# Kernel optimization log

Hardware: AMD Instinct MI355X
Metric: run time of the kernel (lower is better)

The kernel has to match this reference:

```python
import jax, jax.numpy as jnp
import numpy as np

N = 100000
E = 1250000
D = 64
R = 16


def _glorot(key, shape):
    fan_in, fan_out = shape[-2], shape[-1]
    lim = jnp.sqrt(6.0 / (fan_in + fan_out))
    return jax.random.uniform(key, shape, jnp.float32, -lim, lim)


def setup_inputs() -> dict:
    key = jax.random.key(0)
    ks = jax.random.split(key, 9)
    x = jax.random.normal(ks[0], (N, D), jnp.float32)
    edge_index = jax.random.randint(ks[1], (2, E), 0, N, jnp.int64 if jax.config.jax_enable_x64 else jnp.int32).astype(jnp.int32)
    edge_type = jax.random.randint(ks[2], (E,), 0, R).astype(jnp.int32)
    return {
        "x": x,
        "edge_index": edge_index,
        "edge_type": edge_type,
        "W1": _glorot(ks[3], (R, D, D)),
        "sw1": _glorot(ks[4], (D, D)),
        "b1": jnp.zeros((D,), jnp.float32),
        "W2": _glorot(ks[5], (R, D, D)),
        "sw2": _glorot(ks[6], (D, D)),
        "b2": jnp.zeros((D,), jnp.float32),
    }


def _rgcn_layer(x, src, dst, edge_type, W, sw, b, residual):
    # self transform [N, O]
    out = x @ sw
    # per-relation transform of all nodes: [N, R, O] (avoids [E, D, O] gathered weights,
    # same math as bmm(x_j, W[edge_type]))
    xW = jnp.einsum('nd,rdo->nro', x, W)
    msg = xW[src, edge_type]                      # [E, O] per-edge messages
    agg = jax.ops.segment_sum(msg, dst, num_segments=N)  # scatter-add aggregate
    out = out + agg
    if residual:
        out = out + x  # Identity residual (in == out channels)
    out = out + b
    return jax.nn.relu(out)


def reference(x, edge_index, edge_type, W1, sw1, b1, W2, sw2, b2):
    src, dst = edge_index[0], edge_index[1]
    # layer 1: residual=True; layer 2: encoding=False -> no residual.
    # activation (relu) applied after every layer by RGCN.forward; dropout p=0 / eval -> no-op.
    h = _rgcn_layer(x, src, dst, edge_type, W1, sw1, b1, residual=True)
    h = _rgcn_layer(h, src, dst, edge_type, W2, sw2, b2, residual=False)
    return h
```

## Files before the change

kernel.cpp:

```cpp
#include <hip/hip_runtime.h>
#include <hip/hip_bf16.h>

#define NN 100000
#define NE 1250000
#define DD 64
#define RR 16
#define NTILE 6250
#define NBINS 100000
#define NBLK_SCAN 391
#define EBCAP 512

typedef __attribute__((ext_vector_type(8))) short s16x8;
typedef __attribute__((ext_vector_type(4))) float f32x4;

static __device__ __forceinline__ unsigned short f2bf(float v) {
    __hip_bfloat16 h = __float2bfloat16(v);
    return __builtin_bit_cast(unsigned short, h);
}
static __device__ __forceinline__ unsigned int pack2(float a, float b) {
    return ((unsigned int)f2bf(b) << 16) | (unsigned int)f2bf(a);
}


__global__ void hist_key(const int* __restrict__ dst, const int* __restrict__ et,
                         int* __restrict__ cnt) {
    int e = blockIdx.x * 256 + threadIdx.x;
    if (e < NE) atomicAdd(&cnt[(dst[e] >> 4) * 16 + et[e]], 1);
}

__global__ __launch_bounds__(256) void scan1(const int* __restrict__ cnt,
                                             int* __restrict__ rp, int* __restrict__ part) {
    __shared__ int s[256];
    int i = blockIdx.x * 256 + threadIdx.x;
    int v = (i < NBINS) ? cnt[i] : 0;
    s[threadIdx.x] = v;
    __syncthreads();
    for (int off = 1; off < 256; off <<= 1) {
        int t = (threadIdx.x >= off) ? s[threadIdx.x - off] : 0;
        __syncthreads();
        s[threadIdx.x] += t;
        __syncthreads();
    }
    if (i < NBINS) rp[i] = s[threadIdx.x] - v;
    if (threadIdx.x == 255) part[blockIdx.x] = s[255];
}

__global__ void scan2(int* __restrict__ part, int* __restrict__ rp) {
    __shared__ int s[NBLK_SCAN];
    if (threadIdx.x < NBLK_SCAN) s[threadIdx.x] = part[threadIdx.x];
    __syncthreads();
    if (threadIdx.x == 0) {
        int acc = 0;
        for (int b = 0; b < NBLK_SCAN; ++b) { int t = s[b]; s[b] = acc; acc += t; }
        rp[NBINS] = NE;
    }
    __syncthreads();
    if (threadIdx.x < NBLK_SCAN) part[threadIdx.x] = s[threadIdx.x];
}

__global__ void scan3(int* __restrict__ rp, const int* __restrict__ part, int* __restrict__ cur) {
    int i = blockIdx.x * 256 + threadIdx.x;
    if (i < NBINS) {
        int v = rp[i] + part[blockIdx.x];
        rp[i] = v;
        cur[i] = v;
    }
}

__global__ void scatter_key(const int* __restrict__ src, const int* __restrict__ dst,
                            const int* __restrict__ et, int* __restrict__ cur,
                            unsigned int* __restrict__ ep) {
    int e = blockIdx.x * 256 + threadIdx.x;
    if (e >= NE) return;
    int d = dst[e];
    int p = atomicAdd(&cur[(d >> 4) * 16 + et[e]], 1);
    ep[p] = (unsigned int)src[e] | ((unsigned int)(d & 15) << 20);
}


__global__ void prep_w2(const float* __restrict__ W1, const float* __restrict__ sw1,
                        const float* __restrict__ W2, const float* __restrict__ sw2,
                        unsigned short* __restrict__ wt) {
    int i = blockIdx.x * 256 + threadIdx.x;
    if (i >= 2 * 17 * DD * DD) return;
    int d = i & 63;
    int o = (i >> 6) & 63;
    int p = (i >> 12) % 17;
    int l = i / (17 * DD * DD);
    const float* srcp;
    if (p < 16) srcp = (l ? W2 : W1) + p * DD * DD;
    else        srcp = (l ? sw2 : sw1);
    wt[i] = f2bf(srcp[d * DD + o]);
}

__global__ void prep_x2(const float* __restrict__ x, unsigned short* __restrict__ xb) {
    int i = blockIdx.x * blockDim.x + threadIdx.x;
    if (i < NN * DD) xb[i] = f2bf(x[i]);
}

__global__ __launch_bounds__(256) void fused_layer(
    const unsigned short* __restrict__ xb,
    const unsigned short* __restrict__ wt,
    const int* __restrict__ rp,
    const unsigned int* __restrict__ ep,
    const float* __restrict__ bias,
    const float* __restrict__ xres,
    unsigned short* __restrict__ outb,
    float* __restrict__ outf)
{
    __shared__ unsigned int eb[EBCAP];
    __shared__ int rps[17];
    __shared__ float Dred[4 * 1024];
    const int tid  = threadIdx.x;
    const int wid  = tid >> 6;
    const int lane = tid & 63;
    const int c = lane & 15;
    const int q = lane >> 4;
    const int tile = blockIdx.x;
    const int n0 = tile * 16;

    if (tid < 17) rps[tid] = rp[tile * 16 + tid];
    __syncthreads();
    const int e0 = rps[0];
    const int cntT = rps[16] - e0;
    const bool inLds = (cntT <= EBCAP);
    const int nst = min(cntT, EBCAP);
    for (int i = tid; i < nst; i += 256) eb[i] = ep[e0 + i];
    __syncthreads();

    f32x4 D[4];
    #pragma unroll
    for (int ob = 0; ob < 4; ++ob) D[ob] = (f32x4){0.f, 0.f, 0.f, 0.f};

    for (int r = wid; r < 17; r += 4) {
        const unsigned short* wp = wt + r * (DD * DD);
        int s0, s1;
        if (r < 16) { s0 = rps[r]; s1 = rps[r + 1]; } else { s0 = 0; s1 = 16; }

        for (int b0 = s0; b0 < s1; b0 += 32) {
            const int rem = s1 - b0;
            int srcA, dlA;
            if (r < 16) {
                int eA = min(b0 + c, s1 - 1);
                unsigned int wa = inLds ? eb[eA - e0] : ep[eA];
                srcA = (int)(wa & 0xFFFFF);
                dlA  = (b0 + c < s1) ? (int)(wa >> 20) : 31;
            } else { srcA = n0 + c; dlA = c; }
            const bool hasB = (rem > 16);
            int srcB = srcA, dlB = 31;
            if (hasB) {
                int eB = min(b0 + 16 + c, s1 - 1);
                unsigned int wb = inLds ? eb[eB - e0] : ep[eB];
                srcB = (int)(wb & 0xFFFFF);
                dlB  = (b0 + 16 + c < s1) ? (int)(wb >> 20) : 31;
            }

            const unsigned short* xrA = xb + (size_t)srcA * DD + q * 8;
            s16x8 aA0 = *(const s16x8*)(xrA);
            s16x8 aA1 = *(const s16x8*)(xrA + 32);
            s16x8 aB0, aB1;
            if (hasB) {
                const unsigned short* xrB = xb + (size_t)srcB * DD + q * 8;
                aB0 = *(const s16x8*)(xrB);
                aB1 = *(const s16x8*)(xrB + 32);
            }

            s16x8 a2;
            #pragma unroll
            for (int j = 0; j < 4; ++j) {
                int dj = __shfl(dlA, q * 4 + j, 64);
                a2[j] = (dj == c) ? (short)0x3F80 : (short)0;
            }
            if (hasB) {
                #pragma unroll
                for (int j = 0; j < 4; ++j) {
                    int dj = __shfl(dlB, q * 4 + j, 64);
                    a2[j + 4] = (dj == c) ? (short)0x3F80 : (short)0;
                }
            } else {
                #pragma unroll
                for (int j = 0; j < 4; ++j) a2[j + 4] = 0;
            }

            #pragma unroll
            for (int ob = 0; ob < 4; ++ob) {
                const unsigned short* wrow = wp + (ob * 16 + c) * DD + q * 8;
                s16x8 w0 = *(const s16x8*)(wrow);
                s16x8 w1 = *(const s16x8*)(wrow + 32);
                f32x4 cA = {0.f, 0.f, 0.f, 0.f};
                cA = __builtin_amdgcn_mfma_f32_16x16x32_bf16(aA0, w0, cA, 0, 0, 0);
                cA = __builtin_amdgcn_mfma_f32_16x16x32_bf16(aA1, w1, cA, 0, 0, 0);
                s16x8 b2;
                if (hasB) {
                    f32x4 cB = {0.f, 0.f, 0.f, 0.f};
                    cB = __builtin_amdgcn_mfma_f32_16x16x32_bf16(aB0, w0, cB, 0, 0, 0);
                    cB = __builtin_amdgcn_mfma_f32_16x16x32_bf16(aB1, w1, cB, 0, 0, 0);
                    #pragma unroll
                    for (int j = 0; j < 4; ++j) {
                        b2[j]     = (short)f2bf(cA[j]);
                        b2[j + 4] = (short)f2bf(cB[j]);
                    }
                } else {
                    #pragma unroll
                    for (int j = 0; j < 4; ++j) {
                        b2[j]     = (short)f2bf(cA[j]);
                        b2[j + 4] = 0;
                    }
                }
                D[ob] = __builtin_amdgcn_mfma_f32_16x16x32_bf16(a2, b2, D[ob], 0, 0, 0);
            }
        }
    }

    {
        float* dred = Dred + wid * 1024;
        #pragma unroll
        for (int ob = 0; ob < 4; ++ob)
            #pragma unroll
            for (int v = 0; v < 4; ++v)
                dred[(q * 4 + v) * 64 + ob * 16 + c] = D[ob][v];
    }
    __syncthreads();

    #pragma unroll
    for (int k = 0; k < 2; ++k) {
        int j = k * 512 + tid * 2;
        int node = j >> 6, ch = j & 63;
        float v0 = Dred[j]        + Dred[1024 + j]     + Dred[2048 + j]     + Dred[3072 + j];
        float v1 = Dred[j + 1]    + Dred[1024 + j + 1] + Dred[2048 + j + 1] + Dred[3072 + j + 1];
        v0 += bias[ch];
        v1 += bias[ch + 1];
        if (xres) {
            const float2 rv = *(const float2*)(xres + (size_t)(n0 + node) * DD + ch);
            v0 += rv.x; v1 += rv.y;
        }
        v0 = fmaxf(v0, 0.f);
        v1 = fmaxf(v1, 0.f);
        if (outb)
            *(unsigned int*)(outb + (size_t)(n0 + node) * DD + ch) = pack2(v0, v1);
        if (outf) {
            float2 o = {v0, v1};
            *(float2*)(outf + (size_t)(n0 + node) * DD + ch) = o;
        }
    }
}


extern "C" void kernel_launch(void* const* d_in, const int* in_sizes, int n_in,
                              void* d_out, int out_size, void* d_ws, size_t ws_size,
                              hipStream_t stream)
{
    (void)in_sizes; (void)n_in; (void)out_size; (void)ws_size;
    const float* x    = (const float*)d_in[0];
    const int*   ei   = (const int*)d_in[1];
    const int*   et   = (const int*)d_in[2];
    const float* W1   = (const float*)d_in[3];
    const float* sw1  = (const float*)d_in[4];
    const float* b1   = (const float*)d_in[5];
    const float* W2   = (const float*)d_in[6];
    const float* sw2  = (const float*)d_in[7];
    const float* b2   = (const float*)d_in[8];
    float* out = (float*)d_out;

    const int* srcA = ei;
    const int* dstA = ei + NE;

    char* ws = (char*)d_ws;
    unsigned short* xb   = (unsigned short*)(ws);
    unsigned short* h1b  = (unsigned short*)(ws + 12800000);
    unsigned short* wt2  = (unsigned short*)(ws + 25600000);
    unsigned int*   ep   = (unsigned int*)(ws + 25878528);
    int*            rp   = (int*)(ws + 30878528);
    int*            cnt  = (int*)(ws + 31278544);
    int*            cur  = (int*)(ws + 31678544);
    int*            part = (int*)(ws + 32078544);

    const int NB_E    = (NE + 255) / 256;
    const int NB_ELEM = (NN * DD + 255) / 256;
    const int WPL = 17 * DD * DD;

    hipMemsetAsync(cnt, 0, NBINS * sizeof(int), stream);
    hist_key<<<NB_E, 256, 0, stream>>>(dstA, et, cnt);
    scan1<<<NBLK_SCAN, 256, 0, stream>>>(cnt, rp, part);
    scan2<<<1, 512, 0, stream>>>(part, rp);
    scan3<<<NBLK_SCAN, 256, 0, stream>>>(rp, part, cur);
    scatter_key<<<NB_E, 256, 0, stream>>>(srcA, dstA, et, cur, ep);

    prep_w2<<<(2 * 17 * DD * DD + 255) / 256, 256, 0, stream>>>(W1, sw1, W2, sw2, wt2);
    prep_x2<<<NB_ELEM, 256, 0, stream>>>(x, xb);

    fused_layer<<<NTILE, 256, 0, stream>>>(xb, wt2, rp, ep, b1, x, h1b, nullptr);
    fused_layer<<<NTILE, 256, 0, stream>>>(h1b, wt2 + WPL, rp, ep, b2, nullptr, nullptr, out);
}
```

Before: 491.4 us.

## Split output columns across waves and stage gathered source rows in LDS

```diff
diff --git a/kernel.cpp b/kernel.cpp
--- a/kernel.cpp
+++ b/kernel.cpp
@@ -8,6 +8,7 @@
 #define NTILE 6250
 #define NBINS 100000
 #define NBLK_SCAN 391
+#define XCAP 320
 #define EBCAP 512
 
 typedef __attribute__((ext_vector_type(8))) short s16x8;
@@ -108,9 +109,10 @@
     unsigned short* __restrict__ outb,
     float* __restrict__ outf)
 {
+    __shared__ unsigned short xs[XCAP * 72];
     __shared__ unsigned int eb[EBCAP];
+    __shared__ float osg[16 * 65];
     __shared__ int rps[17];
-    __shared__ float Dred[4 * 1024];
     const int tid  = threadIdx.x;
     const int wid  = tid >> 6;
     const int lane = tid & 63;
@@ -122,125 +124,176 @@
     if (tid < 17) rps[tid] = rp[tile * 16 + tid];
     __syncthreads();
     const int e0 = rps[0];
-    const int cntT = rps[16] - e0;
-    const bool inLds = (cntT <= EBCAP);
-    const int nst = min(cntT, EBCAP);
+    const int cnt = rps[16] - e0;
+    const bool useLds = (cnt <= XCAP);
+    const int nst = min(cnt, EBCAP);
+
     for (int i = tid; i < nst; i += 256) eb[i] = ep[e0 + i];
     __syncthreads();
 
-    f32x4 D[4];
-    #pragma unroll
-    for (int ob = 0; ob < 4; ++ob) D[ob] = (f32x4){0.f, 0.f, 0.f, 0.f};
-
-    for (int r = wid; r < 17; r += 4) {
-        const unsigned short* wp = wt + r * (DD * DD);
-        int s0, s1;
-        if (r < 16) { s0 = rps[r]; s1 = rps[r + 1]; } else { s0 = 0; s1 = 16; }
+    if (useLds) {
+        const int npc = cnt * 8;
+        for (int p = tid; p < npc; p += 256) {
+            const int row = p >> 3, j = p & 7;
+            const int s = (int)(eb[row] & 0xFFFFF);
+            s16x8 v = *(const s16x8*)(xb + (size_t)s * DD + j * 8);
+            *(s16x8*)(xs + row * 72 + (j & 3) * 16 + (j >> 2) * 8) = v;
+        }
+    }
+    __syncthreads();
+
+    f32x4 D = {0.f, 0.f, 0.f, 0.f};
+    const int nstm1 = (cnt > 0) ? (cnt - 1) : 0;
+
+    for (int r = 0; r < 16; ++r) {
+        const int s0 = rps[r];
+        const int s1 = (r < 15) ? rps[r + 1] : (e0 + cnt);
+        if (s0 >= s1) continue;
+        const unsigned short* wrow = wt + r * (DD * DD) + (wid * 16 + c) * DD + q * 8;
+        s16x8 w0 = *(const s16x8*)(wrow);
+        s16x8 w1 = *(const s16x8*)(wrow + 32);
 
         for (int b0 = s0; b0 < s1; b0 += 32) {
+            const int lb = b0 - e0;
             const int rem = s1 - b0;
-            int srcA, dlA;
-            if (r < 16) {
-                int eA = min(b0 + c, s1 - 1);
-                unsigned int wa = inLds ? eb[eA - e0] : ep[eA];
-                srcA = (int)(wa & 0xFFFFF);
-                dlA  = (b0 + c < s1) ? (int)(wa >> 20) : 31;
-            } else { srcA = n0 + c; dlA = c; }
             const bool hasB = (rem > 16);
-            int srcB = srcA, dlB = 31;
-            if (hasB) {
-                int eB = min(b0 + 16 + c, s1 - 1);
-                unsigned int wb = inLds ? eb[eB - e0] : ep[eB];
-                srcB = (int)(wb & 0xFFFFF);
-                dlB  = (b0 + 16 + c < s1) ? (int)(wb >> 20) : 31;
-            }
-
-            const unsigned short* xrA = xb + (size_t)srcA * DD + q * 8;
-            s16x8 aA0 = *(const s16x8*)(xrA);
-            s16x8 aA1 = *(const s16x8*)(xrA + 32);
-            s16x8 aB0, aB1;
-            if (hasB) {
-                const unsigned short* xrB = xb + (size_t)srcB * DD + q * 8;
-                aB0 = *(const s16x8*)(xrB);
-                aB1 = *(const s16x8*)(xrB + 32);
-            }
-
+
+            s16x8 aA0, aA1, aB0, aB1;
             s16x8 a2;
-            #pragma unroll
-            for (int j = 0; j < 4; ++j) {
-                int dj = __shfl(dlA, q * 4 + j, 64);
-                a2[j] = (dj == c) ? (short)0x3F80 : (short)0;
-            }
-            if (hasB) {
-                #pragma unroll
-                for (int j = 0; j < 4; ++j) {
-                    int dj = __shfl(dlB, q * 4 + j, 64);
-                    a2[j + 4] = (dj == c) ? (short)0x3F80 : (short)0;
-                }
-            } else {
-                #pragma unroll
-                for (int j = 0; j < 4; ++j) a2[j + 4] = 0;
-            }
-
-            #pragma unroll
-            for (int ob = 0; ob < 4; ++ob) {
-                const unsigned short* wrow = wp + (ob * 16 + c) * DD + q * 8;
-                s16x8 w0 = *(const s16x8*)(wrow);
-                s16x8 w1 = *(const s16x8*)(wrow + 32);
-                f32x4 cA = {0.f, 0.f, 0.f, 0.f};
-                cA = __builtin_amdgcn_mfma_f32_16x16x32_bf16(aA0, w0, cA, 0, 0, 0);
-                cA = __builtin_amdgcn_mfma_f32_16x16x32_bf16(aA1, w1, cA, 0, 0, 0);
-                s16x8 b2;
+            if (useLds) {
+                #pragma unroll
+                for (int j = 0; j < 4; ++j) {
+                    int idx = lb + q * 4 + j;
+                    int dl = (b0 + q * 4 + j < s1) ? (int)(eb[min(idx, nstm1)] >> 20) : 31;
+                    a2[j] = (dl == c) ? (short)0x3F80 : (short)0;
+                }
                 if (hasB) {
-                    f32x4 cB = {0.f, 0.f, 0.f, 0.f};
-                    cB = __builtin_amdgcn_mfma_f32_16x16x32_bf16(aB0, w0, cB, 0, 0, 0);
-                    cB = __builtin_amdgcn_mfma_f32_16x16x32_bf16(aB1, w1, cB, 0, 0, 0);
                     #pragma unroll
                     for (int j = 0; j < 4; ++j) {
-                        b2[j]     = (short)f2bf(cA[j]);
-                        b2[j + 4] = (short)f2bf(cB[j]);
+                        int idx = lb + 16 + q * 4 + j;
+                        int dl = (b0 + 16 + q * 4 + j < s1) ? (int)(eb[min(idx, nstm1)] >> 20) : 31;
+                        a2[j + 4] = (dl == c) ? (short)0x3F80 : (short)0;
                     }
                 } else {
                     #pragma unroll
-                    for (int j = 0; j < 4; ++j) {
-                        b2[j]     = (short)f2bf(cA[j]);
-                        b2[j + 4] = 0;
-                    }
-                }
-                D[ob] = __builtin_amdgcn_mfma_f32_16x16x32_bf16(a2, b2, D[ob], 0, 0, 0);
+                    for (int j = 0; j < 4; ++j) a2[j + 4] = 0;
+                }
+                const unsigned short* rbA = xs + min(lb + c, nstm1) * 72 + q * 16;
+                aA0 = *(const s16x8*)(rbA);
+                aA1 = *(const s16x8*)(rbA + 8);
+                if (hasB) {
+                    const unsigned short* rbB = xs + min(lb + 16 + c, nstm1) * 72 + q * 16;
+                    aB0 = *(const s16x8*)(rbB);
+                    aB1 = *(const s16x8*)(rbB + 8);
+                }
+            } else {
+                int eA = min(b0 + c, s1 - 1);
+                unsigned int wa = ep[eA];
+                int srcA = (int)(wa & 0xFFFFF);
+                int dlA  = (b0 + c < s1) ? (int)(wa >> 20) : 31;
+                int srcB = srcA, dlB = 31;
+                if (hasB) {
+                    int eB = min(b0 + 16 + c, s1 - 1);
+                    unsigned int wb = ep[eB];
+                    srcB = (int)(wb & 0xFFFFF);
+                    dlB  = (b0 + 16 + c < s1) ? (int)(wb >> 20) : 31;
+                }
+                const unsigned short* xrA = xb + (size_t)srcA * DD + q * 8;
+                aA0 = *(const s16x8*)(xrA);
+                aA1 = *(const s16x8*)(xrA + 32);
+                if (hasB) {
+                    const unsigned short* xrB = xb + (size_t)srcB * DD + q * 8;
+                    aB0 = *(const s16x8*)(xrB);
+                    aB1 = *(const s16x8*)(xrB + 32);
+                }
+                #pragma unroll
+                for (int j = 0; j < 4; ++j) {
+                    int dj = __shfl(dlA, q * 4 + j, 64);
+                    a2[j] = (dj == c) ? (short)0x3F80 : (short)0;
+                }
+                #pragma unroll
+                for (int j = 0; j < 4; ++j) {
+                    int dj = hasB ? __shfl(dlB, q * 4 + j, 64) : 31;
+                    a2[j + 4] = (dj == c) ? (short)0x3F80 : (short)0;
+                }
             }
+
+            f32x4 cA = {0.f, 0.f, 0.f, 0.f};
+            cA = __builtin_amdgcn_mfma_f32_16x16x32_bf16(aA0, w0, cA, 0, 0, 0);
+            cA = __builtin_amdgcn_mfma_f32_16x16x32_bf16(aA1, w1, cA, 0, 0, 0);
+            s16x8 b2;
+            if (hasB) {
+                f32x4 cB = {0.f, 0.f, 0.f, 0.f};
+                cB = __builtin_amdgcn_mfma_f32_16x16x32_bf16(aB0, w0, cB, 0, 0, 0);
+                cB = __builtin_amdgcn_mfma_f32_16x16x32_bf16(aB1, w1, cB, 0, 0, 0);
+                #pragma unroll
+                for (int j = 0; j < 4; ++j) {
+                    b2[j]     = (short)f2bf(cA[j]);
+                    b2[j + 4] = (short)f2bf(cB[j]);
+                }
+            } else {
+                #pragma unroll
+                for (int j = 0; j < 4; ++j) {
+                    b2[j]     = (short)f2bf(cA[j]);
+                    b2[j + 4] = 0;
+                }
+            }
+            D = __builtin_amdgcn_mfma_f32_16x16x32_bf16(a2, b2, D, 0, 0, 0);
         }
     }
 
     {
-        float* dred = Dred + wid * 1024;
+        const unsigned short* wrow = wt + 16 * (DD * DD) + (wid * 16 + c) * DD + q * 8;
+        s16x8 w0 = *(const s16x8*)(wrow);
+        s16x8 w1 = *(const s16x8*)(wrow + 32);
+        const unsigned short* xr = xb + (size_t)(n0 + c) * DD + q * 8;
+        s16x8 a0 = *(const s16x8*)(xr);
+        s16x8 a1 = *(const s16x8*)(xr + 32);
+        f32x4 cA = {0.f, 0.f, 0.f, 0.f};
+        cA = __builtin_amdgcn_mfma_f32_16x16x32_bf16(a0, w0, cA, 0, 0, 0);
+        cA = __builtin_amdgcn_mfma_f32_16x16x32_bf16(a1, w1, cA, 0, 0, 0);
+        s16x8 b2;
+        s16x8 a2;
         #pragma unroll
-        for (int ob = 0; ob < 4; ++ob)
-            #pragma unroll
-            for (int v = 0; v < 4; ++v)
-                dred[(q * 4 + v) * 64 + ob * 16 + c] = D[ob][v];
-    }
-    __syncthreads();
+        for (int j = 0; j < 4; ++j) {
+            b2[j]     = (short)f2bf(cA[j]);
+            b2[j + 4] = 0;
+            a2[j]     = (q * 4 + j == c) ? (short)0x3F80 : (short)0;
+            a2[j + 4] = 0;
+        }
+        D = __builtin_amdgcn_mfma_f32_16x16x32_bf16(a2, b2, D, 0, 0, 0);
+    }
 
     #pragma unroll
-    for (int k = 0; k < 2; ++k) {
-        int j = k * 512 + tid * 2;
-        int node = j >> 6, ch = j & 63;
-        float v0 = Dred[j]        + Dred[1024 + j]     + Dred[2048 + j]     + Dred[3072 + j];
-        float v1 = Dred[j + 1]    + Dred[1024 + j + 1] + Dred[2048 + j + 1] + Dred[3072 + j + 1];
-        v0 += bias[ch];
-        v1 += bias[ch + 1];
+    for (int v = 0; v < 4; ++v)
+        osg[(q * 4 + v) * 65 + wid * 16 + c] = D[v];
+    __syncthreads();
+
+    {
+        const int j0 = tid * 4;
+        const int node = j0 >> 6;
+        const int ch = j0 & 63;
+        float v0 = osg[node * 65 + ch];
+        float v1 = osg[node * 65 + ch + 1];
+        float v2 = osg[node * 65 + ch + 2];
+        float v3 = osg[node * 65 + ch + 3];
+        const float4 bv = *(const float4*)(bias + ch);
+        v0 += bv.x; v1 += bv.y; v2 += bv.z; v3 += bv.w;
         if (xres) {
-            const float2 rv = *(const float2*)(xres + (size_t)(n0 + node) * DD + ch);
-            v0 += rv.x; v1 += rv.y;
-        }
-        v0 = fmaxf(v0, 0.f);
-        v1 = fmaxf(v1, 0.f);
-        if (outb)
-            *(unsigned int*)(outb + (size_t)(n0 + node) * DD + ch) = pack2(v0, v1);
+            const float4 rv = *(const float4*)(xres + (size_t)(n0 + node) * DD + ch);
+            v0 += rv.x; v1 += rv.y; v2 += rv.z; v3 += rv.w;
+        }
+        v0 = fmaxf(v0, 0.f); v1 = fmaxf(v1, 0.f);
+        v2 = fmaxf(v2, 0.f); v3 = fmaxf(v3, 0.f);
+        if (outb) {
+            uint2 pk;
+            pk.x = pack2(v0, v1);
+            pk.y = pack2(v2, v3);
+            *(uint2*)(outb + (size_t)(n0 + node) * DD + ch) = pk;
+        }
         if (outf) {
-            float2 o = {v0, v1};
-            *(float2*)(outf + (size_t)(n0 + node) * DD + ch) = o;
+            float4 o = {v0, v1, v2, v3};
+            *(float4*)(outf + (size_t)(n0 + node) * DD + ch) = o;
         }
     }
 }
```

New measurement: 536.1 us. 9.1% more time.

## Software-pipeline edge-chunk gathers with a per-wave chunk list

Applied to the files above, without the earlier changes.

```diff
diff --git a/kernel.cpp b/kernel.cpp
--- a/kernel.cpp
+++ b/kernel.cpp
@@ -9,6 +9,7 @@
 #define NBINS 100000
 #define NBLK_SCAN 391
 #define EBCAP 512
+#define CLCAP 24
 
 typedef __attribute__((ext_vector_type(8))) short s16x8;
 typedef __attribute__((ext_vector_type(4))) float f32x4;
@@ -98,6 +99,82 @@
     if (i < NN * DD) xb[i] = f2bf(x[i]);
 }
 
+
+static __device__ __forceinline__ void load_chunk(
+    const unsigned short* __restrict__ xb,
+    const unsigned int* __restrict__ esrc, int ebase,
+    int b0, int s1, int c, int q,
+    s16x8& aA0, s16x8& aA1, s16x8& aB0, s16x8& aB1,
+    int& dlA, int& dlB, bool& hasB)
+{
+    hasB = (s1 - b0) > 16;
+    int eA = min(b0 + c, s1 - 1);
+    unsigned int wa = esrc[eA - ebase];
+    int srcA = (int)(wa & 0xFFFFF);
+    dlA = (b0 + c < s1) ? (int)(wa >> 20) : 31;
+    const unsigned short* xrA = xb + (size_t)srcA * DD + q * 8;
+    aA0 = *(const s16x8*)(xrA);
+    aA1 = *(const s16x8*)(xrA + 32);
+    dlB = 31;
+    if (hasB) {
+        int eB = min(b0 + 16 + c, s1 - 1);
+        unsigned int wb = esrc[eB - ebase];
+        int srcB = (int)(wb & 0xFFFFF);
+        dlB = (b0 + 16 + c < s1) ? (int)(wb >> 20) : 31;
+        const unsigned short* xrB = xb + (size_t)srcB * DD + q * 8;
+        aB0 = *(const s16x8*)(xrB);
+        aB1 = *(const s16x8*)(xrB + 32);
+    } else {
+        aB0 = aA0;
+        aB1 = aA1;
+    }
+}
+
+static __device__ __forceinline__ void compute_chunk4(
+    const unsigned short* __restrict__ wt, int r, int c, int q,
+    const s16x8& aA0, const s16x8& aA1, const s16x8& aB0, const s16x8& aB1,
+    int dlA, int dlB, bool hasB, f32x4* D)
+{
+    s16x8 a2;
+    #pragma unroll
+    for (int j = 0; j < 4; ++j) {
+        int dj = __shfl(dlA, q * 4 + j, 64);
+        a2[j] = (dj == c) ? (short)0x3F80 : (short)0;
+    }
+    #pragma unroll
+    for (int j = 0; j < 4; ++j) {
+        int dj = hasB ? __shfl(dlB, q * 4 + j, 64) : 31;
+        a2[j + 4] = (dj == c) ? (short)0x3F80 : (short)0;
+    }
+    #pragma unroll
+    for (int ob = 0; ob < 4; ++ob) {
+        const unsigned short* wrow = wt + r * (DD * DD) + (ob * 16 + c) * DD + q * 8;
+        s16x8 w0 = *(const s16x8*)(wrow);
+        s16x8 w1 = *(const s16x8*)(wrow + 32);
+        f32x4 cA = {0.f, 0.f, 0.f, 0.f};
+        cA = __builtin_amdgcn_mfma_f32_16x16x32_bf16(aA0, w0, cA, 0, 0, 0);
+        cA = __builtin_amdgcn_mfma_f32_16x16x32_bf16(aA1, w1, cA, 0, 0, 0);
+        s16x8 b2;
+        if (hasB) {
+            f32x4 cB = {0.f, 0.f, 0.f, 0.f};
+            cB = __builtin_amdgcn_mfma_f32_16x16x32_bf16(aB0, w0, cB, 0, 0, 0);
+            cB = __builtin_amdgcn_mfma_f32_16x16x32_bf16(aB1, w1, cB, 0, 0, 0);
+            #pragma unroll
+            for (int j = 0; j < 4; ++j) {
+                b2[j]     = (short)f2bf(cA[j]);
+                b2[j + 4] = (short)f2bf(cB[j]);
+            }
+        } else {
+            #pragma unroll
+            for (int j = 0; j < 4; ++j) {
+                b2[j]     = (short)f2bf(cA[j]);
+                b2[j + 4] = 0;
+            }
+        }
+        D[ob] = __builtin_amdgcn_mfma_f32_16x16x32_bf16(a2, b2, D[ob], 0, 0, 0);
+    }
+}
+
 __global__ __launch_bounds__(256) void fused_layer(
     const unsigned short* __restrict__ xb,
     const unsigned short* __restrict__ wt,
@@ -111,6 +188,8 @@
     __shared__ unsigned int eb[EBCAP];
     __shared__ int rps[17];
     __shared__ float Dred[4 * 1024];
+    __shared__ int clist[4][CLCAP];
+    __shared__ int cmeta[4][3];
     const int tid  = threadIdx.x;
     const int wid  = tid >> 6;
     const int lane = tid & 63;
@@ -119,96 +198,105 @@
     const int tile = blockIdx.x;
     const int n0 = tile * 16;
 
+    const int e0 = rp[tile * 16];
+    const int cnt = rp[tile * 16 + 16] - e0;
     if (tid < 17) rps[tid] = rp[tile * 16 + tid];
-    __syncthreads();
-    const int e0 = rps[0];
-    const int cntT = rps[16] - e0;
-    const bool inLds = (cntT <= EBCAP);
-    const int nst = min(cntT, EBCAP);
-    for (int i = tid; i < nst; i += 256) eb[i] = ep[e0 + i];
-    __syncthreads();
-
+    const bool inLds = (cnt <= EBCAP);
+    {
+        const int nst = min(cnt, EBCAP);
+        for (int i = tid; i < nst; i += 256) eb[i] = ep[e0 + i];
+    }
+    __syncthreads();
+
+    if (lane == 0) {
+        int m = 0;
+        int ovr = -1, ovb = 0;
+        for (int rr = wid; rr < 16 && ovr < 0; rr += 4) {
+            for (int b0 = rps[rr]; b0 < rps[rr + 1]; b0 += 32) {
+                if (m < CLCAP) clist[wid][m++] = (rr << 27) | (b0 - e0);
+                else { ovr = rr; ovb = b0; break; }
+            }
+        }
+        cmeta[wid][0] = m;
+        cmeta[wid][1] = ovr;
+        cmeta[wid][2] = ovb;
+    }
+    __syncthreads();
+
+    const unsigned int* esrc = inLds ? eb : (ep + e0);
     f32x4 D[4];
     #pragma unroll
     for (int ob = 0; ob < 4; ++ob) D[ob] = (f32x4){0.f, 0.f, 0.f, 0.f};
-
-    for (int r = wid; r < 17; r += 4) {
-        const unsigned short* wp = wt + r * (DD * DD);
-        int s0, s1;
-        if (r < 16) { s0 = rps[r]; s1 = rps[r + 1]; } else { s0 = 0; s1 = 16; }
-
-        for (int b0 = s0; b0 < s1; b0 += 32) {
-            const int rem = s1 - b0;
-            int srcA, dlA;
-            if (r < 16) {
-                int eA = min(b0 + c, s1 - 1);
-                unsigned int wa = inLds ? eb[eA - e0] : ep[eA];
-                srcA = (int)(wa & 0xFFFFF);
-                dlA  = (b0 + c < s1) ? (int)(wa >> 20) : 31;
-            } else { srcA = n0 + c; dlA = c; }
-            const bool hasB = (rem > 16);
-            int srcB = srcA, dlB = 31;
-            if (hasB) {
-                int eB = min(b0 + 16 + c, s1 - 1);
-                unsigned int wb = inLds ? eb[eB - e0] : ep[eB];
-                srcB = (int)(wb & 0xFFFFF);
-                dlB  = (b0 + 16 + c < s1) ? (int)(wb >> 20) : 31;
-            }
-
-            const unsigned short* xrA = xb + (size_t)srcA * DD + q * 8;
-            s16x8 aA0 = *(const s16x8*)(xrA);
-            s16x8 aA1 = *(const s16x8*)(xrA + 32);
-            s16x8 aB0, aB1;
-            if (hasB) {
-                const unsigned short* xrB = xb + (size_t)srcB * DD + q * 8;
-                aB0 = *(const s16x8*)(xrB);
-                aB1 = *(const s16x8*)(xrB + 32);
-            }
-
-            s16x8 a2;
+    const int m = cmeta[wid][0];
+
+    s16x8 aA0, aA1, aB0, aB1;
+    int dlA = 31, dlB = 31;
+    bool hB = false;
+    int rC = 0;
+    if (m > 0) {
+        int meta = clist[wid][0];
+        rC = meta >> 27;
+        int b0 = e0 + (meta & 0x7FFFFFF);
+        load_chunk(xb, esrc, e0, b0, rps[rC + 1], c, q, aA0, aA1, aB0, aB1, dlA, dlB, hB);
+    }
+    for (int ci = 0; ci < m; ++ci) {
+        s16x8 nA0, nA1, nB0, nB1;
+        int ndlA = 31, ndlB = 31;
+        bool nhB = false;
+        int rN = 0;
+        if (ci + 1 < m) {
+            int meta = clist[wid][ci + 1];
+            rN = meta >> 27;
+            int b0 = e0 + (meta & 0x7FFFFFF);
+            load_chunk(xb, esrc, e0, b0, rps[rN + 1], c, q, nA0, nA1, nB0, nB1, ndlA, ndlB, nhB);
+        }
+        compute_chunk4(wt, rC, c, q, aA0, aA1, aB0, aB1, dlA, dlB, hB, D);
+        aA0 = nA0; aA1 = nA1; aB0 = nB0; aB1 = nB1;
+        dlA = ndlA; dlB = ndlB; hB = nhB; rC = rN;
+    }
+
+    {
+        const int orr = cmeta[wid][1];
+        if (orr >= 0) {
+            for (int rr = orr; rr < 16; rr += 4) {
+                const int bst = (rr == orr) ? cmeta[wid][2] : rps[rr];
+                const int s1 = rps[rr + 1];
+                for (int b0 = bst; b0 < s1; b0 += 32) {
+                    s16x8 tA0, tA1, tB0, tB1;
+                    int tdlA, tdlB;
+                    bool thB;
+                    load_chunk(xb, esrc, e0, b0, s1, c, q, tA0, tA1, tB0, tB1, tdlA, tdlB, thB);
+                    compute_chunk4(wt, rr, c, q, tA0, tA1, tB0, tB1, tdlA, tdlB, thB, D);
+                }
+            }
+        }
+    }
+
+    if (wid == 0) {
+        const unsigned short* xr = xb + (size_t)(n0 + c) * DD + q * 8;
+        s16x8 a0 = *(const s16x8*)(xr);
+        s16x8 a1 = *(const s16x8*)(xr + 32);
+        s16x8 a2;
+        #pragma unroll
+        for (int j = 0; j < 4; ++j) {
+            a2[j]     = (q * 4 + j == c) ? (short)0x3F80 : (short)0;
+            a2[j + 4] = 0;
+        }
+        #pragma unroll
+        for (int ob = 0; ob < 4; ++ob) {
+            const unsigned short* wrow = wt + 16 * (DD * DD) + (ob * 16 + c) * DD + q * 8;
+            s16x8 w0 = *(const s16x8*)(wrow);
+            s16x8 w1 = *(const s16x8*)(wrow + 32);
+            f32x4 cA = {0.f, 0.f, 0.f, 0.f};
+            cA = __builtin_amdgcn_mfma_f32_16x16x32_bf16(a0, w0, cA, 0, 0, 0);
+            cA = __builtin_amdgcn_mfma_f32_16x16x32_bf16(a1, w1, cA, 0, 0, 0);
+            s16x8 b2;
             #pragma unroll
             for (int j = 0; j < 4; ++j) {
-                int dj = __shfl(dlA, q * 4 + j, 64);
-                a2[j] = (dj == c) ? (short)0x3F80 : (short)0;
-            }
-            if (hasB) {
-                #pragma unroll
-                for (int j = 0; j < 4; ++j) {
-                    int dj = __shfl(dlB, q * 4 + j, 64);
-                    a2[j + 4] = (dj == c) ? (short)0x3F80 : (short)0;
-                }
-            } else {
-                #pragma unroll
-                for (int j = 0; j < 4; ++j) a2[j + 4] = 0;
-            }
-
-            #pragma unroll
-            for (int ob = 0; ob < 4; ++ob) {
-                const unsigned short* wrow = wp + (ob * 16 + c) * DD + q * 8;
-                s16x8 w0 = *(const s16x8*)(wrow);
-                s16x8 w1 = *(const s16x8*)(wrow + 32);
-                f32x4 cA = {0.f, 0.f, 0.f, 0.f};
-                cA = __builtin_amdgcn_mfma_f32_16x16x32_bf16(aA0, w0, cA, 0, 0, 0);
-                cA = __builtin_amdgcn_mfma_f32_16x16x32_bf16(aA1, w1, cA, 0, 0, 0);
-                s16x8 b2;
-                if (hasB) {
-                    f32x4 cB = {0.f, 0.f, 0.f, 0.f};
-                    cB = __builtin_amdgcn_mfma_f32_16x16x32_bf16(aB0, w0, cB, 0, 0, 0);
-                    cB = __builtin_amdgcn_mfma_f32_16x16x32_bf16(aB1, w1, cB, 0, 0, 0);
-                    #pragma unroll
-                    for (int j = 0; j < 4; ++j) {
-                        b2[j]     = (short)f2bf(cA[j]);
-                        b2[j + 4] = (short)f2bf(cB[j]);
-                    }
-                } else {
-                    #pragma unroll
-                    for (int j = 0; j < 4; ++j) {
-                        b2[j]     = (short)f2bf(cA[j]);
-                        b2[j + 4] = 0;
-                    }
-                }
-                D[ob] = __builtin_amdgcn_mfma_f32_16x16x32_bf16(a2, b2, D[ob], 0, 0, 0);
-            }
+                b2[j]     = (short)f2bf(cA[j]);
+                b2[j + 4] = 0;
+            }
+            D[ob] = __builtin_amdgcn_mfma_f32_16x16x32_bf16(a2, b2, D[ob], 0, 0, 0);
         }
     }
 
```

After: 530.0 us. 7.9% more time.
